# Optimization experiments

Measured on AMD Instinct MI355X. Metric: run time of the kernel, lower is better.

## Reference

```python
import jax, jax.numpy as jnp
import numpy as np

GAMMA = 1.0  # kernel_gamma

def setup_inputs() -> dict:
    key = jax.random.key(0)
    ks = jax.random.split(key, 8)
    B, T, D, P, H = 32, 512, 256, 512, 512
    return {
        "x": jax.random.normal(ks[0], (B, T, D), dtype=jnp.float32),
        "prototypes": jax.random.normal(ks[1], (P, D), dtype=jnp.float32),
        "W_lin": jax.random.normal(ks[2], (H, P), dtype=jnp.float32) * (1.0 / np.sqrt(P)),
        "b_lin": jax.random.normal(ks[3], (H,), dtype=jnp.float32) * 0.01,
        "W_ih": jax.random.normal(ks[4], (4 * H, H), dtype=jnp.float32) * (1.0 / np.sqrt(H)),
        "W_hh": jax.random.normal(ks[5], (4 * H, H), dtype=jnp.float32) * (1.0 / np.sqrt(H)),
        "b_ih": jax.random.normal(ks[6], (4 * H,), dtype=jnp.float32) * 0.01,
        "b_hh": jax.random.normal(ks[7], (4 * H,), dtype=jnp.float32) * 0.01,
    }

def _rbf(x_flat, prototypes):
    x2 = jnp.sum(x_flat * x_flat, axis=-1, keepdims=True)          # (N, 1)
    p2 = jnp.sum(prototypes * prototypes, axis=-1)                  # (P,)
    sq = x2 + p2[None, :] - 2.0 * (x_flat @ prototypes.T)           # (N, P)
    return jnp.exp(-GAMMA * jnp.maximum(sq, 0.0))

def _lstm(feats, W_ih, W_hh, b_ih, b_hh):
    # feats: (B, T, H); torch gate order i, f, g, o; zero initial state
    B, T, H = feats.shape
    xs = jnp.einsum('bth,gh->tbg', feats, W_ih) + (b_ih + b_hh)     # (T, B, 4H)

    def step(carry, x_t):
        h, c = carry
        gates = x_t + h @ W_hh.T                                     # (B, 4H)
        i, f, g, o = jnp.split(gates, 4, axis=-1)
        i, f, o = jax.nn.sigmoid(i), jax.nn.sigmoid(f), jax.nn.sigmoid(o)
        g = jnp.tanh(g)
        c = f * c + i * g
        h = o * jnp.tanh(c)
        return (h, c), h

    h0 = jnp.zeros((B, H), dtype=feats.dtype)
    c0 = jnp.zeros((B, H), dtype=feats.dtype)
    _, hs = jax.lax.scan(step, (h0, c0), xs)                         # hs: (T, B, H)
    return jnp.transpose(hs, (1, 0, 2))                              # (B, T, H)

def reference(x, prototypes, W_lin, b_lin, W_ih, W_hh, b_ih, b_hh):
    B, T, D = x.shape
    feats = _rbf(x.reshape(B * T, D), prototypes)                    # (B*T, P)
    feats = feats.reshape(B, T, -1) @ W_lin.T + b_lin                # (B, T, H)
    return _lstm(feats, W_ih, W_hh, b_ih, b_hh)
```

## Files before the change

### kernel.cpp

```cpp
#include <hip/hip_runtime.h>

#define Bb 32
#define Tt 512
#define Dd 256
#define Pp 512
#define Hh 512
#define G4 2048
#define TC 128
#define NG 8
#define WPG 16
#define NBG 4

__device__ __forceinline__ float sigmf(float x){ return 1.0f/(1.0f+__expf(-x)); }
__device__ __forceinline__ float tanhf_(float x){ return 1.0f - 2.0f/(__expf(2.0f*x)+1.0f); }

__global__ void k_rowsq(const float* __restrict__ A, float* __restrict__ o, int M, int K){
  int m = blockIdx.x*blockDim.x + threadIdx.x;
  if (m >= M) return;
  const float4* a4 = (const float4*)(A + (size_t)m*K);
  float s = 0.f;
  for (int i = 0; i < K/4; ++i){ float4 v = a4[i]; s += v.x*v.x + v.y*v.y + v.z*v.z + v.w*v.w; }
  o[m] = s;
}

__global__ void k_transpose(const float* __restrict__ in, float* __restrict__ out, int M, int N){
  __shared__ float tile[32][33];
  int bn = blockIdx.x * 32;
  int bm = blockIdx.y * 32;
  int tx = threadIdx.x, ty = threadIdx.y;
  #pragma unroll
  for (int i = 0; i < 32; i += 8)
    tile[ty+i][tx] = in[(size_t)(bm+ty+i)*N + bn+tx];
  __syncthreads();
  #pragma unroll
  for (int i = 0; i < 32; i += 8)
    out[(size_t)(bn+ty+i)*M + bm+tx] = tile[tx][ty+i];
}

__global__ void k_bx(const float* __restrict__ Wih, const float* __restrict__ blin,
                     const float* __restrict__ bih, const float* __restrict__ bhh,
                     float* __restrict__ bx){
  int r = blockIdx.x*blockDim.x + threadIdx.x;
  const float4* w4 = (const float4*)(Wih + (size_t)r*Hh);
  const float4* b4 = (const float4*)blin;
  float s = 0.f;
  for (int i = 0; i < Hh/4; ++i){ float4 w=w4[i], b=b4[i]; s += w.x*b.x+w.y*b.y+w.z*b.z+w.w*b.w; }
  bx[r] = s + bih[r] + bhh[r];
}

template<int EPI, bool REMAP>
__global__ __launch_bounds__(256) void k_gemm(const float* __restrict__ A, const float* __restrict__ Bm,
                                              float* __restrict__ C, int M, int N, int K,
                                              const float* __restrict__ rowAux,
                                              const float* __restrict__ colAux, int t0)
{
  __shared__ float As[16][132];
  __shared__ float Bs[16][68];
  const int tid = threadIdx.x;
  const int bm = blockIdx.x * 128;
  const int bn = blockIdx.y * 64;
  const int tm = (tid & 15) * 8;
  const int tn = (tid >> 4) * 4;
  const int arow = tid >> 1;
  const int akq  = (tid & 1) * 8;
  const int brow = tid >> 4;
  const int bcol = (tid & 15) * 4;
  const int am = bm + arow;
  const size_t aRow = REMAP ? ((size_t)(am >> 7) * Tt + t0 + (am & 127)) : (size_t)am;
  float acc[8][4] = {};
  for (int k0 = 0; k0 < K; k0 += 16){
    float4 a0 = *(const float4*)&A[aRow*K + k0 + akq];
    float4 a1 = *(const float4*)&A[aRow*K + k0 + akq + 4];
    float4 bv = *(const float4*)&Bm[(size_t)(k0 + brow)*N + bn + bcol];
    As[akq+0][arow]=a0.x; As[akq+1][arow]=a0.y; As[akq+2][arow]=a0.z; As[akq+3][arow]=a0.w;
    As[akq+4][arow]=a1.x; As[akq+5][arow]=a1.y; As[akq+6][arow]=a1.z; As[akq+7][arow]=a1.w;
    *(float4*)&Bs[brow][bcol] = bv;
    __syncthreads();
    #pragma unroll
    for (int kk = 0; kk < 16; ++kk){
      float4 x0 = *(const float4*)&As[kk][tm];
      float4 x1 = *(const float4*)&As[kk][tm+4];
      float4 y  = *(const float4*)&Bs[kk][tn];
      float av[8] = {x0.x,x0.y,x0.z,x0.w,x1.x,x1.y,x1.z,x1.w};
      #pragma unroll
      for (int i=0;i<8;++i){
        float a = av[i];
        acc[i][0] += a*y.x; acc[i][1] += a*y.y; acc[i][2] += a*y.z; acc[i][3] += a*y.w;
      }
    }
    __syncthreads();
  }
  #pragma unroll
  for (int i=0;i<8;++i){
    int m = bm + tm + i;
    size_t mAux = REMAP ? ((size_t)(m >> 7) * Tt + t0 + (m & 127)) : (size_t)m;
    float4 o;
    float vv[4];
    #pragma unroll
    for (int j=0;j<4;++j){
      int n = bn + tn + j;
      float v = acc[i][j];
      if (EPI==1)      v = __expf(-fmaxf(rowAux[mAux] + colAux[n] - 2.f*v, 0.f));
      else if (EPI==2) v = v + colAux[n];
      vv[j] = v;
    }
    o.x=vv[0]; o.y=vv[1]; o.z=vv[2]; o.w=vv[3];
    *(float4*)&C[(size_t)m*N + bn + tn] = o;
  }
}

__global__ __launch_bounds__(512, 2) void k_lstm_persist(
    const float* __restrict__ Whh, const float* __restrict__ xs,
    float* __restrict__ cbuf, float* __restrict__ out,
    unsigned* __restrict__ cnt, int t0)
{
  __shared__ float hbuf[NBG*Hh];
  const int tid  = threadIdx.x;
  const int gid  = blockIdx.x & 7;
  const int wg   = blockIdx.x >> 3;
  const int gsel = tid & 3;
  const int ks   = (tid >> 2) & 15;
  const int ug   = tid >> 6;
  const int jbase = wg*32 + ug*4;

  float W[4][32];
  #pragma unroll
  for (int r = 0; r < 4; ++r){
    const float* wrow = &Whh[(size_t)(gsel*Hh + jbase + r)*Hh + ks*32];
    #pragma unroll
    for (int c = 0; c < 8; ++c){
      float4 w = *(const float4*)&wrow[c*4];
      W[r][c*4+0]=w.x; W[r][c*4+1]=w.y; W[r][c*4+2]=w.z; W[r][c*4+3]=w.w;
    }
  }

  const int rr = ks >> 2;
  const int bl = ks & 3;
  const int j  = jbase + rr;
  const int b  = gid*NBG + bl;
  float c_st = (t0 == 0) ? 0.f : cbuf[(size_t)b*Hh + j];

  const int sbl = tid >> 7;
  const int skb = (tid & 127) * 4;
  const int ssw = skb ^ (((skb >> 5) & 7) << 2);

  for (int tl = 0; tl < TC; ++tl){
    const int t = t0 + tl;
    float4 hv = {0.f,0.f,0.f,0.f};
    if (t > 0){
      const float* src = &out[((size_t)(gid*NBG + sbl)*Tt + (t-1))*Hh + skb];
      hv.x = __hip_atomic_load(src+0, __ATOMIC_RELAXED, __HIP_MEMORY_SCOPE_AGENT);
      hv.y = __hip_atomic_load(src+1, __ATOMIC_RELAXED, __HIP_MEMORY_SCOPE_AGENT);
      hv.z = __hip_atomic_load(src+2, __ATOMIC_RELAXED, __HIP_MEMORY_SCOPE_AGENT);
      hv.w = __hip_atomic_load(src+3, __ATOMIC_RELAXED, __HIP_MEMORY_SCOPE_AGENT);
    }
    *(float4*)&hbuf[sbl*Hh + ssw] = hv;
    __syncthreads();

    float acc[4][4];
    #pragma unroll
    for (int r=0;r<4;++r){ acc[r][0]=0.f; acc[r][1]=0.f; acc[r][2]=0.f; acc[r][3]=0.f; }
    #pragma unroll
    for (int blq = 0; blq < 4; ++blq){
      const float* hb = &hbuf[blq*Hh + ks*32];
      #pragma unroll
      for (int c = 0; c < 8; ++c){
        float4 h4 = *(const float4*)&hb[(c*4) ^ ((ks & 7) << 2)];
        #pragma unroll
        for (int r = 0; r < 4; ++r){
          acc[r][blq] = fmaf(W[r][c*4+0], h4.x, acc[r][blq]);
          acc[r][blq] = fmaf(W[r][c*4+1], h4.y, acc[r][blq]);
          acc[r][blq] = fmaf(W[r][c*4+2], h4.z, acc[r][blq]);
          acc[r][blq] = fmaf(W[r][c*4+3], h4.w, acc[r][blq]);
        }
      }
    }

    #pragma unroll
    for (int m = 4; m <= 32; m <<= 1){
      #pragma unroll
      for (int r=0;r<4;++r){
        #pragma unroll
        for (int q=0;q<4;++q)
          acc[r][q] += __shfl_xor(acc[r][q], m, 64);
      }
    }
    float g = acc[0][0];
    #pragma unroll
    for (int r=0;r<4;++r){
      #pragma unroll
      for (int q=0;q<4;++q)
        if (ks == r*4+q) g = acc[r][q];
    }

    g += xs[((size_t)b*TC + tl)*G4 + gsel*Hh + j];
    const int lbase = (tid & 63) & ~3;
    float gi = __shfl(g, lbase+0, 64);
    float gf = __shfl(g, lbase+1, 64);
    float gg = __shfl(g, lbase+2, 64);
    float go = __shfl(g, lbase+3, 64);
    gi = sigmf(gi); gf = sigmf(gf); gg = tanhf_(gg); go = sigmf(go);
    c_st = gf*c_st + gi*gg;
    float h = go * tanhf_(c_st);
    if (gsel == 0)
      __hip_atomic_store(&out[((size_t)b*Tt + t)*Hh + j], h,
                         __ATOMIC_RELAXED, __HIP_MEMORY_SCOPE_AGENT);
    __syncthreads();

    if (tid == 0){
      __hip_atomic_fetch_add(&cnt[gid], 1u, __ATOMIC_RELEASE, __HIP_MEMORY_SCOPE_AGENT);
      const unsigned tgt = (unsigned)WPG * (unsigned)(t + 1);
      while (__hip_atomic_load(&cnt[gid], __ATOMIC_ACQUIRE, __HIP_MEMORY_SCOPE_AGENT) < tgt)
        __builtin_amdgcn_s_sleep(1);
    }
    __syncthreads();
  }
  if (gsel == 0) cbuf[(size_t)b*Hh + j] = c_st;
}

extern "C" void kernel_launch(void* const* d_in, const int* in_sizes, int n_in,
                              void* d_out, int out_size, void* d_ws, size_t ws_size,
                              hipStream_t stream)
{
  const float* x    = (const float*)d_in[0];
  const float* prot = (const float*)d_in[1];
  const float* Wlin = (const float*)d_in[2];
  const float* blin = (const float*)d_in[3];
  const float* Wih  = (const float*)d_in[4];
  const float* Whh  = (const float*)d_in[5];
  const float* bih  = (const float*)d_in[6];
  const float* bhh  = (const float*)d_in[7];
  float* out = (float*)d_out;
  float* ws  = (float*)d_ws;

  size_t off = 0;
  auto alloc = [&](size_t n)->float*{ float* p = ws + off; off += (n + 15) & ~((size_t)15); return p; };
  float* x2    = alloc((size_t)Bb*Tt);
  float* p2    = alloc(Pp);
  float* pT    = alloc((size_t)Dd*Pp);
  float* bx    = alloc(G4);
  float* Wx    = alloc((size_t)G4*Pp);
  float* WxT   = alloc((size_t)Pp*G4);
  float* cbuf  = alloc((size_t)Bb*Hh);
  float* featsC= alloc((size_t)Bb*TC*Pp);
  float* xsC   = alloc((size_t)Bb*TC*G4);
  unsigned* cnt = (unsigned*)alloc(16);

  k_rowsq<<<dim3((Bb*Tt)/256), dim3(256), 0, stream>>>(x, x2, Bb*Tt, Dd);
  k_rowsq<<<dim3(Pp/256), dim3(256), 0, stream>>>(prot, p2, Pp, Dd);
  k_transpose<<<dim3(Dd/32, Pp/32), dim3(32,8), 0, stream>>>(prot, pT, Pp, Dd);
  k_bx<<<dim3(G4/256), dim3(256), 0, stream>>>(Wih, blin, bih, bhh, bx);
  k_gemm<0,false><<<dim3(G4/128, Pp/64), dim3(256), 0, stream>>>(Wih, Wlin, Wx, G4, Pp, Hh, nullptr, nullptr, 0);
  k_transpose<<<dim3(Pp/32, G4/32), dim3(32,8), 0, stream>>>(Wx, WxT, G4, Pp);
  hipMemsetAsync(cnt, 0, NG*sizeof(unsigned), stream);

  for (int ch = 0; ch < Tt/TC; ++ch){
    int t0 = ch * TC;
    k_gemm<1,true><<<dim3((Bb*TC)/128, Pp/64), dim3(256), 0, stream>>>(
        x, pT, featsC, Bb*TC, Pp, Dd, x2, p2, t0);
    k_gemm<2,false><<<dim3((Bb*TC)/128, G4/64), dim3(256), 0, stream>>>(
        featsC, WxT, xsC, Bb*TC, G4, Pp, nullptr, bx, 0);
    void* args[] = { (void*)&Whh, (void*)&xsC, (void*)&cbuf, (void*)&out, (void*)&cnt, (void*)&t0 };
    hipLaunchCooperativeKernel((void*)k_lstm_persist, dim3(NG*WPG), dim3(512), args, 0, stream);
  }
}
```

Baseline: 3.713 ms.

## Split LSTM recurrence across twice the blocks and use per-block flag barrier

Doubles the number of workgroups per batch group in the persistent LSTM so each block holds only two hidden units' W_hh rows, spreading the recurrent matvec across more CUs. Replaces the shared atomic counter barrier with per-block release flags that a wavefront polls collectively before reading the previous hidden state. This aims to cut per-step compute latency and atomic contention, but half the lanes now do redundant work and each group must synchronise more blocks, with busy polling and no sleep.

```diff
diff --git a/kernel.cpp b/kernel.cpp
--- a/kernel.cpp
+++ b/kernel.cpp
@@ -8,7 +8,7 @@
 #define G4 2048
 #define TC 128
 #define NG 8
-#define WPG 16
+#define WPG 32
 #define NBG 4
 
 __device__ __forceinline__ float sigmf(float x){ return 1.0f/(1.0f+__expf(-x)); }
@@ -112,7 +112,7 @@
 __global__ __launch_bounds__(512, 2) void k_lstm_persist(
     const float* __restrict__ Whh, const float* __restrict__ xs,
     float* __restrict__ cbuf, float* __restrict__ out,
-    unsigned* __restrict__ cnt, int t0)
+    unsigned* __restrict__ flags, int t0)
 {
   __shared__ float hbuf[NBG*Hh];
   const int tid  = threadIdx.x;
@@ -121,11 +121,11 @@
   const int gsel = tid & 3;
   const int ks   = (tid >> 2) & 15;
   const int ug   = tid >> 6;
-  const int jbase = wg*32 + ug*4;
-
-  float W[4][32];
-  #pragma unroll
-  for (int r = 0; r < 4; ++r){
+  const int jbase = wg*16 + ug*2;
+
+  float W[2][32];
+  #pragma unroll
+  for (int r = 0; r < 2; ++r){
     const float* wrow = &Whh[(size_t)(gsel*Hh + jbase + r)*Hh + ks*32];
     #pragma unroll
     for (int c = 0; c < 8; ++c){
@@ -133,10 +133,15 @@
       W[r][c*4+0]=w.x; W[r][c*4+1]=w.y; W[r][c*4+2]=w.z; W[r][c*4+3]=w.w;
     }
   }
+  #pragma unroll
+  for (int r = 0; r < 2; ++r)
+    #pragma unroll
+    for (int c = 0; c < 32; ++c)
+      asm volatile("" : "+v"(W[r][c]));
 
   const int rr = ks >> 2;
   const int bl = ks & 3;
-  const int j  = jbase + rr;
+  const int j  = jbase + (rr & 1);
   const int b  = gid*NBG + bl;
   float c_st = (t0 == 0) ? 0.f : cbuf[(size_t)b*Hh + j];
 
@@ -146,6 +151,17 @@
 
   for (int tl = 0; tl < TC; ++tl){
     const int t = t0 + tl;
+
+    if (t > 0 && tid < 64){
+      const unsigned tgt = (unsigned)t;
+      const unsigned fi = gid*WPG + (tid & (WPG-1));
+      for (;;){
+        unsigned f = __hip_atomic_load(&flags[fi], __ATOMIC_ACQUIRE, __HIP_MEMORY_SCOPE_AGENT);
+        if (__all((int)(f >= tgt))) break;
+      }
+    }
+    __syncthreads();
+
     float4 hv = {0.f,0.f,0.f,0.f};
     if (t > 0){
       const float* src = &out[((size_t)(gid*NBG + sbl)*Tt + (t-1))*Hh + skb];
@@ -157,9 +173,9 @@
     *(float4*)&hbuf[sbl*Hh + ssw] = hv;
     __syncthreads();
 
-    float acc[4][4];
-    #pragma unroll
-    for (int r=0;r<4;++r){ acc[r][0]=0.f; acc[r][1]=0.f; acc[r][2]=0.f; acc[r][3]=0.f; }
+    float acc[2][4];
+    #pragma unroll
+    for (int r=0;r<2;++r){ acc[r][0]=0.f; acc[r][1]=0.f; acc[r][2]=0.f; acc[r][3]=0.f; }
     #pragma unroll
     for (int blq = 0; blq < 4; ++blq){
       const float* hb = &hbuf[blq*Hh + ks*32];
@@ -167,7 +183,7 @@
       for (int c = 0; c < 8; ++c){
         float4 h4 = *(const float4*)&hb[(c*4) ^ ((ks & 7) << 2)];
         #pragma unroll
-        for (int r = 0; r < 4; ++r){
+        for (int r = 0; r < 2; ++r){
           acc[r][blq] = fmaf(W[r][c*4+0], h4.x, acc[r][blq]);
           acc[r][blq] = fmaf(W[r][c*4+1], h4.y, acc[r][blq]);
           acc[r][blq] = fmaf(W[r][c*4+2], h4.z, acc[r][blq]);
@@ -179,7 +195,7 @@
     #pragma unroll
     for (int m = 4; m <= 32; m <<= 1){
       #pragma unroll
-      for (int r=0;r<4;++r){
+      for (int r=0;r<2;++r){
         #pragma unroll
         for (int q=0;q<4;++q)
           acc[r][q] += __shfl_xor(acc[r][q], m, 64);
@@ -187,13 +203,13 @@
     }
     float g = acc[0][0];
     #pragma unroll
-    for (int r=0;r<4;++r){
+    for (int r=0;r<2;++r)
       #pragma unroll
       for (int q=0;q<4;++q)
         if (ks == r*4+q) g = acc[r][q];
-    }
-
-    g += xs[((size_t)b*TC + tl)*G4 + gsel*Hh + j];
+
+    if (ks < 8)
+      g += xs[((size_t)b*TC + tl)*G4 + gsel*Hh + j];
     const int lbase = (tid & 63) & ~3;
     float gi = __shfl(g, lbase+0, 64);
     float gf = __shfl(g, lbase+1, 64);
@@ -202,20 +218,16 @@
     gi = sigmf(gi); gf = sigmf(gf); gg = tanhf_(gg); go = sigmf(go);
     c_st = gf*c_st + gi*gg;
     float h = go * tanhf_(c_st);
-    if (gsel == 0)
+    if (gsel == 0 && ks < 8)
       __hip_atomic_store(&out[((size_t)b*Tt + t)*Hh + j], h,
                          __ATOMIC_RELAXED, __HIP_MEMORY_SCOPE_AGENT);
     __syncthreads();
 
-    if (tid == 0){
-      __hip_atomic_fetch_add(&cnt[gid], 1u, __ATOMIC_RELEASE, __HIP_MEMORY_SCOPE_AGENT);
-      const unsigned tgt = (unsigned)WPG * (unsigned)(t + 1);
-      while (__hip_atomic_load(&cnt[gid], __ATOMIC_ACQUIRE, __HIP_MEMORY_SCOPE_AGENT) < tgt)
-        __builtin_amdgcn_s_sleep(1);
-    }
-    __syncthreads();
-  }
-  if (gsel == 0) cbuf[(size_t)b*Hh + j] = c_st;
+    if (tid == 0)
+      __hip_atomic_store(&flags[gid*WPG + wg], (unsigned)(t + 1),
+                         __ATOMIC_RELEASE, __HIP_MEMORY_SCOPE_AGENT);
+  }
+  if (gsel == 0 && ks < 8) cbuf[(size_t)b*Hh + j] = c_st;
 }
 
 extern "C" void kernel_launch(void* const* d_in, const int* in_sizes, int n_in,
@@ -244,7 +256,7 @@
   float* cbuf  = alloc((size_t)Bb*Hh);
   float* featsC= alloc((size_t)Bb*TC*Pp);
   float* xsC   = alloc((size_t)Bb*TC*G4);
-  unsigned* cnt = (unsigned*)alloc(16);
+  unsigned* flags = (unsigned*)alloc(NG*WPG);
 
   k_rowsq<<<dim3((Bb*Tt)/256), dim3(256), 0, stream>>>(x, x2, Bb*Tt, Dd);
   k_rowsq<<<dim3(Pp/256), dim3(256), 0, stream>>>(prot, p2, Pp, Dd);
@@ -252,7 +264,7 @@
   k_bx<<<dim3(G4/256), dim3(256), 0, stream>>>(Wih, blin, bih, bhh, bx);
   k_gemm<0,false><<<dim3(G4/128, Pp/64), dim3(256), 0, stream>>>(Wih, Wlin, Wx, G4, Pp, Hh, nullptr, nullptr, 0);
   k_transpose<<<dim3(Pp/32, G4/32), dim3(32,8), 0, stream>>>(Wx, WxT, G4, Pp);
-  hipMemsetAsync(cnt, 0, NG*sizeof(unsigned), stream);
+  hipMemsetAsync(flags, 0, NG*WPG*sizeof(unsigned), stream);
 
   for (int ch = 0; ch < Tt/TC; ++ch){
     int t0 = ch * TC;
@@ -260,7 +272,7 @@
         x, pT, featsC, Bb*TC, Pp, Dd, x2, p2, t0);
     k_gemm<2,false><<<dim3((Bb*TC)/128, G4/64), dim3(256), 0, stream>>>(
         featsC, WxT, xsC, Bb*TC, G4, Pp, nullptr, bx, 0);
-    void* args[] = { (void*)&Whh, (void*)&xsC, (void*)&cbuf, (void*)&out, (void*)&cnt, (void*)&t0 };
+    void* args[] = { (void*)&Whh, (void*)&xsC, (void*)&cbuf, (void*)&out, (void*)&flags, (void*)&t0 };
     hipLaunchCooperativeKernel((void*)k_lstm_persist, dim3(NG*WPG), dim3(512), args, 0, stream);
   }
 }
```

New measurement: 5.357 ms. 1.44x slower.

## Compute input-gate projection with bf16 MFMA GEMM instead of fp32 SIMT

Applied to the files above, without the earlier changes.

Replaces the fp32 SIMT GEMM that multiplies the RBF features by the fused W_ih·W_lin weight with a bf16 MFMA kernel (16x16x32 bf16 intrinsic, 128x128 tiles). Features and weights are converted to bf16 with round-to-nearest-even, which drops the weight transpose and adds a conversion pass per chunk. The aim is to speed up the largest per-chunk GEMM using matrix cores. The cost is reduced precision in the gate pre-activations, which then feed a 512-step recurrence.

```diff
diff --git a/kernel.cpp b/kernel.cpp
--- a/kernel.cpp
+++ b/kernel.cpp
@@ -14,6 +14,9 @@
 __device__ __forceinline__ float sigmf(float x){ return 1.0f/(1.0f+__expf(-x)); }
 __device__ __forceinline__ float tanhf_(float x){ return 1.0f - 2.0f/(__expf(2.0f*x)+1.0f); }
 
+typedef __attribute__((ext_vector_type(8))) short v8s;
+typedef __attribute__((ext_vector_type(4))) float f32x4;
+
 __global__ void k_rowsq(const float* __restrict__ A, float* __restrict__ o, int M, int K){
   int m = blockIdx.x*blockDim.x + threadIdx.x;
   if (m >= M) return;
@@ -46,6 +49,19 @@
   float s = 0.f;
   for (int i = 0; i < Hh/4; ++i){ float4 w=w4[i], b=b4[i]; s += w.x*b.x+w.y*b.y+w.z*b.z+w.w*b.w; }
   bx[r] = s + bih[r] + bhh[r];
+}
+
+__global__ void k_cvt_bf16(const float* __restrict__ in, ushort* __restrict__ out, int n4){
+  int i = blockIdx.x*blockDim.x + threadIdx.x;
+  if (i >= n4) return;
+  float4 v = ((const float4*)in)[i];
+  ushort4 o;
+  uint u;
+  u = __float_as_uint(v.x); u += 0x7FFF + ((u>>16)&1); o.x = (ushort)(u>>16);
+  u = __float_as_uint(v.y); u += 0x7FFF + ((u>>16)&1); o.y = (ushort)(u>>16);
+  u = __float_as_uint(v.z); u += 0x7FFF + ((u>>16)&1); o.z = (ushort)(u>>16);
+  u = __float_as_uint(v.w); u += 0x7FFF + ((u>>16)&1); o.w = (ushort)(u>>16);
+  ((ushort4*)out)[i] = o;
 }
 
 template<int EPI, bool REMAP>
@@ -100,12 +116,73 @@
     for (int j=0;j<4;++j){
       int n = bn + tn + j;
       float v = acc[i][j];
-      if (EPI==1)      v = __expf(-fmaxf(rowAux[mAux] + colAux[n] - 2.f*v, 0.f));
-      else if (EPI==2) v = v + colAux[n];
+      if (EPI==1) v = __expf(-fmaxf(rowAux[mAux] + colAux[n] - 2.f*v, 0.f));
       vv[j] = v;
     }
     o.x=vv[0]; o.y=vv[1]; o.z=vv[2]; o.w=vv[3];
     *(float4*)&C[(size_t)m*N + bn + tn] = o;
+  }
+}
+
+__global__ __launch_bounds__(256) void k_xs_mfma(
+    const ushort* __restrict__ A, const ushort* __restrict__ Bm,
+    const float* __restrict__ bx, float* __restrict__ C, int M, int N, int K)
+{
+  __shared__ ushort As[128][72];
+  __shared__ ushort Ws[128][72];
+  const int tid  = threadIdx.x;
+  const int bm   = blockIdx.x * 128;
+  const int bn   = blockIdx.y * 128;
+  const int lane = tid & 63;
+  const int w    = tid >> 6;
+  const int wr   = w >> 1, wc = w & 1;
+  const int srow = tid >> 1;
+  const int scol = (tid & 1) * 32;
+  const int fr   = lane & 15;
+  const int fk   = (lane >> 4) * 8;
+
+  f32x4 acc[4][4] = {};
+
+  for (int k0 = 0; k0 < K; k0 += 64){
+    const ushort* ag = &A [(size_t)(bm + srow)*K + k0 + scol];
+    const ushort* wg = &Bm[(size_t)(bn + srow)*K + k0 + scol];
+    #pragma unroll
+    for (int q = 0; q < 4; ++q){
+      *(v8s*)&As[srow][scol + q*8] = *(const v8s*)&ag[q*8];
+      *(v8s*)&Ws[srow][scol + q*8] = *(const v8s*)&wg[q*8];
+    }
+    __syncthreads();
+    #pragma unroll
+    for (int kk = 0; kk < 64; kk += 32){
+      v8s af[4], bf[4];
+      #pragma unroll
+      for (int mi = 0; mi < 4; ++mi)
+        af[mi] = *(const v8s*)&As[wr*64 + mi*16 + fr][kk + fk];
+      #pragma unroll
+      for (int ni = 0; ni < 4; ++ni)
+        bf[ni] = *(const v8s*)&Ws[wc*64 + ni*16 + fr][kk + fk];
+      #pragma unroll
+      for (int mi = 0; mi < 4; ++mi)
+        #pragma unroll
+        for (int ni = 0; ni < 4; ++ni)
+          acc[mi][ni] = __builtin_amdgcn_mfma_f32_16x16x32_bf16(af[mi], bf[ni], acc[mi][ni], 0, 0, 0);
+    }
+    __syncthreads();
+  }
+
+  const int cr = lane >> 4;
+  #pragma unroll
+  for (int ni = 0; ni < 4; ++ni){
+    const int n = bn + wc*64 + ni*16 + fr;
+    const float bb = bx[n];
+    #pragma unroll
+    for (int mi = 0; mi < 4; ++mi){
+      #pragma unroll
+      for (int r = 0; r < 4; ++r){
+        const int m = bm + wr*64 + mi*16 + cr*4 + r;
+        C[(size_t)m*N + n] = acc[mi][ni][r] + bb;
+      }
+    }
   }
 }
 
@@ -235,15 +312,16 @@
 
   size_t off = 0;
   auto alloc = [&](size_t n)->float*{ float* p = ws + off; off += (n + 15) & ~((size_t)15); return p; };
-  float* x2    = alloc((size_t)Bb*Tt);
-  float* p2    = alloc(Pp);
-  float* pT    = alloc((size_t)Dd*Pp);
-  float* bx    = alloc(G4);
-  float* Wx    = alloc((size_t)G4*Pp);
-  float* WxT   = alloc((size_t)Pp*G4);
-  float* cbuf  = alloc((size_t)Bb*Hh);
-  float* featsC= alloc((size_t)Bb*TC*Pp);
-  float* xsC   = alloc((size_t)Bb*TC*G4);
+  float* x2     = alloc((size_t)Bb*Tt);
+  float* p2     = alloc(Pp);
+  float* pT     = alloc((size_t)Dd*Pp);
+  float* bx     = alloc(G4);
+  float* Wx     = alloc((size_t)G4*Pp);
+  ushort* WxB   = (ushort*)alloc((size_t)G4*Pp/2);
+  float* cbuf   = alloc((size_t)Bb*Hh);
+  float* featsC = alloc((size_t)Bb*TC*Pp);
+  ushort* featsB= (ushort*)alloc((size_t)Bb*TC*Pp/2);
+  float* xsC    = alloc((size_t)Bb*TC*G4);
   unsigned* cnt = (unsigned*)alloc(16);
 
   k_rowsq<<<dim3((Bb*Tt)/256), dim3(256), 0, stream>>>(x, x2, Bb*Tt, Dd);
@@ -251,15 +329,16 @@
   k_transpose<<<dim3(Dd/32, Pp/32), dim3(32,8), 0, stream>>>(prot, pT, Pp, Dd);
   k_bx<<<dim3(G4/256), dim3(256), 0, stream>>>(Wih, blin, bih, bhh, bx);
   k_gemm<0,false><<<dim3(G4/128, Pp/64), dim3(256), 0, stream>>>(Wih, Wlin, Wx, G4, Pp, Hh, nullptr, nullptr, 0);
-  k_transpose<<<dim3(Pp/32, G4/32), dim3(32,8), 0, stream>>>(Wx, WxT, G4, Pp);
+  k_cvt_bf16<<<dim3((G4*Pp/4)/256), dim3(256), 0, stream>>>(Wx, WxB, G4*Pp/4);
   hipMemsetAsync(cnt, 0, NG*sizeof(unsigned), stream);
 
   for (int ch = 0; ch < Tt/TC; ++ch){
     int t0 = ch * TC;
     k_gemm<1,true><<<dim3((Bb*TC)/128, Pp/64), dim3(256), 0, stream>>>(
         x, pT, featsC, Bb*TC, Pp, Dd, x2, p2, t0);
-    k_gemm<2,false><<<dim3((Bb*TC)/128, G4/64), dim3(256), 0, stream>>>(
-        featsC, WxT, xsC, Bb*TC, G4, Pp, nullptr, bx, 0);
+    k_cvt_bf16<<<dim3((Bb*TC*Pp/4)/256), dim3(256), 0, stream>>>(featsC, featsB, Bb*TC*Pp/4);
+    k_xs_mfma<<<dim3((Bb*TC)/128, G4/128), dim3(256), 0, stream>>>(
+        featsB, WxB, bx, xsC, Bb*TC, G4, Pp);
     void* args[] = { (void*)&Whh, (void*)&xsC, (void*)&cbuf, (void*)&out, (void*)&cnt, (void*)&t0 };
     hipLaunchCooperativeKernel((void*)k_lstm_persist, dim3(NG*WPG), dim3(512), args, 0, stream);
   }
```

After: 3.395 ms. 1.09x faster.
